# Optimization experiments

Measured on AMD Instinct MI355X. Metric: run time of the kernel, lower is better.

Reference implementation:

```python
import jax, jax.numpy as jnp
import numpy as np
import math

T, B, N, D = 4, 4, 1024, 512
H = 8
HD = D // H
EPS = 1e-6


def setup_inputs() -> dict:
    key = jax.random.key(0)
    ks = jax.random.split(key, 9)
    s = 1.0 / math.sqrt(D)
    inp = {"x": jax.random.normal(ks[0], (T, B, N, D), dtype=jnp.float32)}
    names = ["wq", "wk", "wv", "wo"]
    for i, nm in enumerate(names):
        inp[nm] = jax.random.uniform(ks[1 + i], (D, D), dtype=jnp.float32, minval=-s, maxval=s)
        inp["b" + nm[1]] = jax.random.uniform(ks[5 + i], (D,), dtype=jnp.float32, minval=-s, maxval=s)
    return inp


def reference(x, wq, bq, wk, bk, wv, bv, wo, bo):
    t, b, n, d = x.shape
    # torch Linear: y = x @ W.T + bias
    q = x @ wq.T + bq
    k = x @ wk.T + bk
    v = x @ wv.T + bv
    # (t, b, n, H, HD) -> (t, b, H, n, HD)
    qh = q.reshape(t, b, n, H, HD).transpose(0, 1, 3, 2, 4)
    kh = k.reshape(t, b, n, H, HD).transpose(0, 1, 3, 2, 4)
    vh = v.reshape(t, b, n, H, HD).transpose(0, 1, 3, 2, 4)
    scores = jnp.einsum("tbhqd,tbhkd->tbhqk", qh, kh) / math.sqrt(HD)
    attn = jax.nn.relu(scores)
    attn = attn / (attn.sum(axis=-1, keepdims=True) + EPS)
    ctx = jnp.einsum("tbhqk,tbhkd->tbhqd", attn, vh)
    out = ctx.transpose(0, 1, 3, 2, 4).reshape(t, b, n, d)
    return out @ wo.T + bo
```

## Files before the change

### kernel.cpp

```cpp
#include <hip/hip_runtime.h>

typedef unsigned short u16;
typedef __attribute__((ext_vector_type(8))) short bf16x8;
typedef __attribute__((ext_vector_type(4))) float f32x4;
typedef __attribute__((ext_vector_type(16))) float f32x16;
typedef __attribute__((ext_vector_type(2))) unsigned int u32x2;

__device__ inline u16 f2b(float f) {
    unsigned u;
    __builtin_memcpy(&u, &f, 4);
    unsigned r = u + 0x7FFF + ((u >> 16) & 1);
    return (u16)(r >> 16);
}

__device__ inline bf16x8 pack8(const float* p) {
    union { u16 us[8]; bf16x8 v; } r;
#pragma unroll
    for (int i = 0; i < 8; i++) r.us[i] = f2b(p[i]);
    return r.v;
}

__device__ inline unsigned cvtpk(float lo, float hi) {
    unsigned r;
    asm("v_cvt_pk_bf16_f32 %0, %1, %2" : "=v"(r) : "v"(lo), "v"(hi));
    return r;
}

__device__ inline void gload16(const void* g, void* l) {
    __builtin_amdgcn_global_load_lds((__attribute__((address_space(1))) void*)g,
                                     (__attribute__((address_space(3))) void*)l, 16, 0, 0);
}

__global__ __launch_bounds__(256) void conv_kernel(const float* __restrict__ x,
                                                   const float* __restrict__ wq,
                                                   const float* __restrict__ wk,
                                                   const float* __restrict__ wv,
                                                   const float* __restrict__ wo,
                                                   u16* __restrict__ xb, u16* __restrict__ wb) {
    const int bid = blockIdx.x;
    const float* src;
    u16* dst;
    size_t base;
    if (bid < 4096) {
        src = x; dst = xb; base = (size_t)bid * 2048;
    } else {
        const int wsel = (bid - 4096) >> 7;
        src = (wsel == 0) ? wq : (wsel == 1) ? wk : (wsel == 2) ? wv : wo;
        dst = wb + (size_t)wsel * 262144;
        base = (size_t)((bid - 4096) & 127) * 2048;
    }
    const size_t idx = base + (size_t)threadIdx.x * 8;
    float a[8];
    *(float4*)&a[0] = *(const float4*)&src[idx];
    *(float4*)&a[4] = *(const float4*)&src[idx + 4];
    *(bf16x8*)&dst[idx] = pack8(a);
}

template <int MODE>
__global__ __launch_bounds__(256) void gemm_kernel(const u16* __restrict__ A,
                                                   const u16* __restrict__ W,
                                                   const float* __restrict__ B0,
                                                   const float* __restrict__ B1,
                                                   const float* __restrict__ B2,
                                                   void* __restrict__ O0v, u16* __restrict__ O1,
                                                   u16* __restrict__ O2) {
    const int m0 = blockIdx.x * 128;
    const int n0 = blockIdx.y * 128;
    const int seg = (MODE == 0) ? (n0 >> 9) : 0;
    const int nl0 = (MODE == 0) ? (n0 & 511) : n0;
    const float* Bb = (seg == 0) ? B0 : (seg == 1) ? B1 : B2;
    u16* O = (seg == 0) ? (u16*)O0v : (seg == 1) ? O1 : O2;

    __shared__ __align__(16) u16 Al[128 * 32];
    __shared__ __align__(16) u16 Bl[128 * 32];

    const int tid = threadIdx.x;
    const int lane = tid & 63, wave = tid >> 6;
    const int quad = lane >> 4, col = lane & 15;
    const int wm = wave >> 1, wn = wave & 1;

    f32x4 acc[4][4];
#pragma unroll
    for (int i = 0; i < 4; i++)
#pragma unroll
        for (int j = 0; j < 4; j++) acc[i][j] = (f32x4){0.f, 0.f, 0.f, 0.f};

    for (int k0 = 0; k0 < 512; k0 += 32) {
#pragma unroll
        for (int sh = 0; sh < 4; sh++) {
            const int c = tid + sh * 256;
            const int cl = c & 511;
            const int row = cl >> 2, cc = (cl & 3) * 8;
            if (c < 512)
                gload16(&A[(size_t)(m0 + row) * 512 + k0 + cc], &Al[cl * 8]);
            else
                gload16(&W[(size_t)(n0 + row) * 512 + k0 + cc], &Bl[cl * 8]);
        }
        __syncthreads();
        bf16x8 af[4], bfr[4];
#pragma unroll
        for (int t = 0; t < 4; t++) {
            af[t] = *(const bf16x8*)&Al[(wm * 64 + t * 16 + col) * 32 + quad * 8];
            bfr[t] = *(const bf16x8*)&Bl[(wn * 64 + t * 16 + col) * 32 + quad * 8];
        }
#pragma unroll
        for (int i = 0; i < 4; i++)
#pragma unroll
            for (int j = 0; j < 4; j++)
                acc[i][j] = __builtin_amdgcn_mfma_f32_16x16x32_bf16(af[i], bfr[j], acc[i][j], 0, 0, 0);
        __syncthreads();
    }

    float bias[4];
#pragma unroll
    for (int j = 0; j < 4; j++) bias[j] = Bb[nl0 + wn * 64 + j * 16 + col];

#pragma unroll
    for (int i = 0; i < 4; i++) {
        const int mbase = m0 + wm * 64 + i * 16 + quad * 4;
#pragma unroll
        for (int j = 0; j < 4; j++) {
            const int nl = nl0 + wn * 64 + j * 16 + col;
            if (MODE == 1) {
                float* Of = (float*)O0v;
#pragma unroll
                for (int r = 0; r < 4; r++)
                    Of[(size_t)(mbase + r) * 512 + nl] = acc[i][j][r] + bias[j];
            } else {
                const int h = nl >> 6, hd = nl & 63;
                if (seg < 2) {
                    const float qs = (seg == 0) ? 0.125f : 1.f;
#pragma unroll
                    for (int r = 0; r < 4; r++) {
                        int m = mbase + r;
                        int s = m >> 10, tok = m & 1023;
                        O[(size_t)((s * 8 + h) * 1024 + tok) * 64 + hd] =
                            f2b((acc[i][j][r] + bias[j]) * qs);
                    }
                } else {
                    int s = mbase >> 10, tok0 = mbase & 1023;
                    union { u16 us[4]; uint2 v; } pk;
#pragma unroll
                    for (int r = 0; r < 4; r++) pk.us[r] = f2b(acc[i][j][r] + bias[j]);
                    *(uint2*)&O[(size_t)((s * 8 + h) * 64 + hd) * 1024 + tok0] = pk.v;
                }
            }
        }
    }
}

__global__ __launch_bounds__(256, 2) void attn_kernel(const u16* __restrict__ Q,
                                                      const u16* __restrict__ Kp,
                                                      const u16* __restrict__ Vt,
                                                      u16* __restrict__ Ctx) {
    __shared__ __align__(16) u16 Kl[2][4096];
    __shared__ __align__(16) u16 Vl[2][4096];

    const int bid = blockIdx.x;
    const int head = bid & 127;
    const int qt = bid >> 7;
    const int s = head >> 3, h = head & 7;
    const u16* Qh = Q + (size_t)head * 65536;
    const u16* Kh = Kp + (size_t)head * 65536;
    const u16* Vh = Vt + (size_t)head * 65536;

    const int tid = threadIdx.x;
    const int lane = tid & 63, wave = tid >> 6;
    const int l31 = lane & 31, hi = lane >> 5;
    const int q0 = qt * 256 + wave * 64;
    const int cx = l31 & 7;

    int srow[2], sxc[2];
#pragma unroll
    for (int i = 0; i < 2; i++) {
        const int p = tid + i * 256;
        srow[i] = p >> 3;
        sxc[i] = (p & 7) ^ (srow[i] & 7);
    }

#define STAGE(B, K0)                                                                    \
    {                                                                                   \
        _Pragma("unroll") for (int i_ = 0; i_ < 2; i_++) {                              \
            const int p_ = tid + i_ * 256;                                              \
            gload16(&Kh[(size_t)((K0) + srow[i_]) * 64 + sxc[i_] * 8], &Kl[B][p_ * 8]); \
        }                                                                               \
        _Pragma("unroll") for (int i_ = 0; i_ < 2; i_++) {                              \
            const int p_ = tid + i_ * 256;                                              \
            gload16(&Vh[(size_t)srow[i_] * 1024 + (K0) + sxc[i_] * 8], &Vl[B][p_ * 8]); \
        }                                                                               \
    }

    union { u16 us[8]; bf16x8 v; } one;
#pragma unroll
    for (int i = 0; i < 8; i++) one.us[i] = 0x3F80;
    const bf16x8 onesf = one.v;

    bf16x8 qf[2][4];
#pragma unroll
    for (int q2 = 0; q2 < 2; q2++)
#pragma unroll
        for (int kk = 0; kk < 4; kk++)
            qf[q2][kk] =
                *(const bf16x8*)&Qh[(size_t)(q0 + q2 * 32 + l31) * 64 + kk * 16 + hi * 8];

    f32x16 cacc[2][2];
    f32x16 dacc[2];
#pragma unroll
    for (int q2 = 0; q2 < 2; q2++) {
#pragma unroll
        for (int r = 0; r < 16; r++) {
            cacc[q2][0][r] = 0.f;
            cacc[q2][1][r] = 0.f;
            dacc[q2][r] = 0.f;
        }
    }

    STAGE(0, 0)
    __syncthreads();

    int buf = 0;
    for (int kt = 0; kt < 16; kt++) {
        if (kt < 15) STAGE(buf ^ 1, (kt + 1) * 64)

        bf16x8 pa[2][4];
#pragma unroll
        for (int mt = 0; mt < 2; mt++) {
            f32x16 s0, s1;
#pragma unroll
            for (int r = 0; r < 16; r++) { s0[r] = 0.f; s1[r] = 0.f; }
            __builtin_amdgcn_s_setprio(1);
#pragma unroll
            for (int kk = 0; kk < 4; kk++) {
                const bf16x8 kf =
                    *(const bf16x8*)&Kl[buf][((mt * 32 + l31) * 8 + ((2 * kk + hi) ^ cx)) * 8];
                s0 = __builtin_amdgcn_mfma_f32_32x32x16_bf16(kf, qf[0][kk], s0, 0, 0, 0);
                s1 = __builtin_amdgcn_mfma_f32_32x32x16_bf16(kf, qf[1][kk], s1, 0, 0, 0);
            }
            __builtin_amdgcn_s_setprio(0);

#pragma unroll
            for (int q2 = 0; q2 < 2; q2++) {
                const f32x16& sc = q2 ? s1 : s0;
                const unsigned c0 = cvtpk(fmaxf(sc[0], 0.f), fmaxf(sc[1], 0.f));
                const unsigned c1 = cvtpk(fmaxf(sc[2], 0.f), fmaxf(sc[3], 0.f));
                const unsigned c2 = cvtpk(fmaxf(sc[4], 0.f), fmaxf(sc[5], 0.f));
                const unsigned c3 = cvtpk(fmaxf(sc[6], 0.f), fmaxf(sc[7], 0.f));
                const unsigned c4 = cvtpk(fmaxf(sc[8], 0.f), fmaxf(sc[9], 0.f));
                const unsigned c5 = cvtpk(fmaxf(sc[10], 0.f), fmaxf(sc[11], 0.f));
                const unsigned c6 = cvtpk(fmaxf(sc[12], 0.f), fmaxf(sc[13], 0.f));
                const unsigned c7 = cvtpk(fmaxf(sc[14], 0.f), fmaxf(sc[15], 0.f));
                const u32x2 s02 = __builtin_amdgcn_permlane32_swap(c0, c2, false, false);
                const u32x2 s13 = __builtin_amdgcn_permlane32_swap(c1, c3, false, false);
                const u32x2 s46 = __builtin_amdgcn_permlane32_swap(c4, c6, false, false);
                const u32x2 s57 = __builtin_amdgcn_permlane32_swap(c5, c7, false, false);
                union { unsigned u[4]; bf16x8 v; } f0u, f1u;
                f0u.u[0] = s02.x; f0u.u[1] = s13.x; f0u.u[2] = s02.y; f0u.u[3] = s13.y;
                f1u.u[0] = s46.x; f1u.u[1] = s57.x; f1u.u[2] = s46.y; f1u.u[3] = s57.y;
                pa[q2][mt * 2 + 0] = f0u.v;
                pa[q2][mt * 2 + 1] = f1u.v;
            }
        }

        __builtin_amdgcn_s_setprio(1);
#pragma unroll
        for (int kg = 0; kg < 4; kg++) {
            const bf16x8 vf0 = *(const bf16x8*)&Vl[buf][(l31 * 8 + ((2 * kg + hi) ^ cx)) * 8];
            const bf16x8 vf1 =
                *(const bf16x8*)&Vl[buf][((32 + l31) * 8 + ((2 * kg + hi) ^ cx)) * 8];
            dacc[0] = __builtin_amdgcn_mfma_f32_32x32x16_bf16(pa[0][kg], onesf, dacc[0], 0, 0, 0);
            dacc[1] = __builtin_amdgcn_mfma_f32_32x32x16_bf16(pa[1][kg], onesf, dacc[1], 0, 0, 0);
            cacc[0][0] = __builtin_amdgcn_mfma_f32_32x32x16_bf16(pa[0][kg], vf0, cacc[0][0], 0, 0, 0);
            cacc[0][1] = __builtin_amdgcn_mfma_f32_32x32x16_bf16(pa[0][kg], vf1, cacc[0][1], 0, 0, 0);
            cacc[1][0] = __builtin_amdgcn_mfma_f32_32x32x16_bf16(pa[1][kg], vf0, cacc[1][0], 0, 0, 0);
            cacc[1][1] = __builtin_amdgcn_mfma_f32_32x32x16_bf16(pa[1][kg], vf1, cacc[1][1], 0, 0, 0);
        }
        __builtin_amdgcn_s_setprio(0);

        __syncthreads();
        buf ^= 1;
    }
#undef STAGE

#pragma unroll
    for (int q2 = 0; q2 < 2; q2++) {
#pragma unroll
        for (int r = 0; r < 16; r++) {
            const int ql = (r & 3) + 8 * (r >> 2) + 4 * hi;
            const float inv = 1.f / (dacc[q2][r] + 1e-6f);
            const size_t grow = (size_t)(s * 1024 + q0 + q2 * 32 + ql);
            Ctx[grow * 512 + h * 64 + l31] = f2b(cacc[q2][0][r] * inv);
            Ctx[grow * 512 + h * 64 + 32 + l31] = f2b(cacc[q2][1][r] * inv);
        }
    }
}

extern "C" void kernel_launch(void* const* d_in, const int* in_sizes, int n_in, void* d_out,
                              int out_size, void* d_ws, size_t ws_size, hipStream_t stream) {
    const float* x = (const float*)d_in[0];
    const float* wq = (const float*)d_in[1];
    const float* bq = (const float*)d_in[2];
    const float* wk = (const float*)d_in[3];
    const float* bk = (const float*)d_in[4];
    const float* wv = (const float*)d_in[5];
    const float* bv = (const float*)d_in[6];
    const float* wo = (const float*)d_in[7];
    const float* bo = (const float*)d_in[8];

    const size_t E = 16384ull * 512ull;
    u16* xb = (u16*)d_ws;
    u16* cw = xb;
    u16* wb = xb + E;
    u16* qw = wb + 4 * 262144;
    u16* kw = qw + E;
    u16* vw = kw + E;

    conv_kernel<<<dim3(4096 + 512), 256, 0, stream>>>(x, wq, wk, wv, wo, xb, wb);
    gemm_kernel<0><<<dim3(128, 12), 256, 0, stream>>>(xb, wb, bq, bk, bv, qw, kw, vw);
    attn_kernel<<<dim3(512), 256, 0, stream>>>(qw, kw, vw, cw);
    gemm_kernel<1><<<dim3(128, 4), 256, 0, stream>>>(cw, wb + 3 * 262144, bo, nullptr, nullptr,
                                                     d_out, nullptr, nullptr);
}
```

Baseline: 197.7 us.

## Double-buffer GEMM LDS tiles with XOR swizzle and MFMA priority boost

The projection GEMM now keeps two LDS buffers, so the next K-slice is loaded from global memory while MFMAs run on the current one, and the loop needs only one barrier per iteration. The global-to-LDS addressing swaps chunk positions with an XOR pattern to cut LDS bank conflicts on fragment reads. It also raises wave priority around the MFMA block. The cost is twice the shared memory, which may lower occupancy.

Measured after the change: 191.0 us. -3.4%, faster.

```diff
diff --git a/kernel.cpp b/kernel.cpp
--- a/kernel.cpp
+++ b/kernel.cpp
@@ -71,45 +71,65 @@
     const float* Bb = (seg == 0) ? B0 : (seg == 1) ? B1 : B2;
     u16* O = (seg == 0) ? (u16*)O0v : (seg == 1) ? O1 : O2;
 
-    __shared__ __align__(16) u16 Al[128 * 32];
-    __shared__ __align__(16) u16 Bl[128 * 32];
+    __shared__ __align__(16) u16 Al[2][128 * 32];
+    __shared__ __align__(16) u16 Bl[2][128 * 32];
 
     const int tid = threadIdx.x;
     const int lane = tid & 63, wave = tid >> 6;
     const int quad = lane >> 4, col = lane & 15;
     const int wm = wave >> 1, wn = wave & 1;
 
+    int srow[2], ssc[2];
+#pragma unroll
+    for (int i = 0; i < 2; i++) {
+        const int cl = tid + i * 256;
+        srow[i] = cl >> 2;
+        ssc[i] = (((cl & 3) ^ ((srow[i] >> 1) & 3))) * 8;
+    }
+    const int cswz = quad ^ ((col >> 1) & 3);
+
+#define GSTAGE(BUF, K0)                                                                   \
+    {                                                                                     \
+        _Pragma("unroll") for (int i_ = 0; i_ < 2; i_++) {                                \
+            const int cl_ = tid + i_ * 256;                                               \
+            gload16(&A[(size_t)(m0 + srow[i_]) * 512 + (K0) + ssc[i_]], &Al[BUF][cl_ * 8]); \
+        }                                                                                 \
+        _Pragma("unroll") for (int i_ = 0; i_ < 2; i_++) {                                \
+            const int cl_ = tid + i_ * 256;                                               \
+            gload16(&W[(size_t)(n0 + srow[i_]) * 512 + (K0) + ssc[i_]], &Bl[BUF][cl_ * 8]); \
+        }                                                                                 \
+    }
+
     f32x4 acc[4][4];
 #pragma unroll
     for (int i = 0; i < 4; i++)
 #pragma unroll
         for (int j = 0; j < 4; j++) acc[i][j] = (f32x4){0.f, 0.f, 0.f, 0.f};
 
+    GSTAGE(0, 0)
+    __syncthreads();
+
+    int bufi = 0;
     for (int k0 = 0; k0 < 512; k0 += 32) {
-#pragma unroll
-        for (int sh = 0; sh < 4; sh++) {
-            const int c = tid + sh * 256;
-            const int cl = c & 511;
-            const int row = cl >> 2, cc = (cl & 3) * 8;
-            if (c < 512)
-                gload16(&A[(size_t)(m0 + row) * 512 + k0 + cc], &Al[cl * 8]);
-            else
-                gload16(&W[(size_t)(n0 + row) * 512 + k0 + cc], &Bl[cl * 8]);
-        }
-        __syncthreads();
+        if (k0 < 480) GSTAGE(bufi ^ 1, k0 + 32)
+
         bf16x8 af[4], bfr[4];
 #pragma unroll
         for (int t = 0; t < 4; t++) {
-            af[t] = *(const bf16x8*)&Al[(wm * 64 + t * 16 + col) * 32 + quad * 8];
-            bfr[t] = *(const bf16x8*)&Bl[(wn * 64 + t * 16 + col) * 32 + quad * 8];
-        }
+            af[t] = *(const bf16x8*)&Al[bufi][((wm * 64 + t * 16 + col) * 4 + cswz) * 8];
+            bfr[t] = *(const bf16x8*)&Bl[bufi][((wn * 64 + t * 16 + col) * 4 + cswz) * 8];
+        }
+        __builtin_amdgcn_s_setprio(1);
 #pragma unroll
         for (int i = 0; i < 4; i++)
 #pragma unroll
             for (int j = 0; j < 4; j++)
                 acc[i][j] = __builtin_amdgcn_mfma_f32_16x16x32_bf16(af[i], bfr[j], acc[i][j], 0, 0, 0);
+        __builtin_amdgcn_s_setprio(0);
         __syncthreads();
-    }
+        bufi ^= 1;
+    }
+#undef GSTAGE
 
     float bias[4];
 #pragma unroll
```
